# Optimization experiments

Hardware: AMD Instinct MI355X
Metric: run time of the kernel (lower is better)

## Reference

```python
import jax, jax.numpy as jnp
from jax import lax
import numpy as np

HF, WF, CIN, CONV_C, A, STRIDE = 100, 160, 512, 512, 9, 16
NEG = -1e9
IOU_THR = 0.7


def _make_anchor_map(hf, wf, stride):
    # (cy, cx, h, w) per anchor, 9 anchors: scales {64,128,256} x ratios {0.5,1,2}
    cy = (np.arange(hf, dtype=np.float32) + 0.5) * stride
    cx = (np.arange(wf, dtype=np.float32) + 0.5) * stride
    sizes = np.array([[s * np.sqrt(r), s / np.sqrt(r)]
                      for s in (64.0, 128.0, 256.0) for r in (0.5, 1.0, 2.0)],
                     dtype=np.float32)  # [9,2] = (h,w)
    cyg, cxg = np.meshgrid(cy, cx, indexing='ij')  # [hf,wf]
    am = np.zeros((hf, wf, A, 4), np.float32)
    am[..., 0] = cyg[..., None]
    am[..., 1] = cxg[..., None]
    am[..., 2] = sizes[:, 0]
    am[..., 3] = sizes[:, 1]
    return jnp.asarray(am.reshape(1, hf, wf, 4 * A))


def _conv(x, w, b, pad):
    y = lax.conv_general_dilated(x, w, (1, 1), pad,
                                 dimension_numbers=('NHWC', 'HWIO', 'NHWC'))
    return y + b


def _nms(boxes, scores, max_out, iou_thr):
    # jit-friendly fixed-size NMS; index computation is non-differentiable.
    bx = lax.stop_gradient(boxes)
    y1, x1, y2, x2 = bx[:, 0], bx[:, 1], bx[:, 2], bx[:, 3]
    areas = (y2 - y1) * (x2 - x1)

    def step(sc, _):
        best = jnp.argmax(sc)
        ok = sc[best] > NEG * 0.5
        b = bx[best]
        iy1 = jnp.maximum(y1, b[0]); ix1 = jnp.maximum(x1, b[1])
        iy2 = jnp.minimum(y2, b[2]); ix2 = jnp.minimum(x2, b[3])
        inter = jnp.maximum(iy2 - iy1, 0.0) * jnp.maximum(ix2 - ix1, 0.0)
        iou = inter / (areas + areas[best] - inter + 1e-8)
        sc = jnp.where((iou > iou_thr) & ok, NEG, sc)
        sc = sc.at[best].set(NEG)
        return sc, (best, ok)

    _, (keep, valid) = lax.scan(step, lax.stop_gradient(scores), None, length=max_out)
    return jnp.where(valid[:, None], boxes[keep], 0.0)  # [max_out,4], zero-padded


def setup_inputs() -> dict:
    key = jax.random.key(0)
    ks = jax.random.split(key, 6)
    image = jax.random.normal(ks[0], (1, HF * STRIDE, WF * STRIDE, 3), jnp.float32)
    feature_map = jax.random.normal(ks[1], (1, HF, WF, CIN), jnp.float32)
    anchor_map = _make_anchor_map(HF, WF, STRIDE)
    W1 = jax.random.normal(ks[2], (3, 3, CIN, CONV_C), jnp.float32) * 0.01
    b1 = jnp.zeros((CONV_C,), jnp.float32)
    Wc = jax.random.normal(ks[3], (1, 1, CONV_C, A), jnp.float32) * 0.01
    bc = jnp.zeros((A,), jnp.float32)
    Wr = jax.random.normal(ks[4], (1, 1, CONV_C, 4 * A), jnp.float32) * 0.01
    br = jnp.zeros((4 * A,), jnp.float32)
    return {'image': image, 'feature_map': feature_map, 'anchor_map': anchor_map,
            'W1': W1, 'b1': b1, 'Wc': Wc, 'bc': bc, 'Wr': Wr, 'br': br, 'training': 0}


def reference(image, feature_map, anchor_map, W1, b1, Wc, bc, Wr, br, training):
    pre_nms, post_nms = ((12000, 2000) if training else (6000, 300))
    # conv heads
    y = jax.nn.relu(_conv(feature_map, W1, b1, 'SAME'))
    scores_map = jax.nn.softmax(_conv(y, Wc, bc, 'SAME'), axis=-1)   # [1,HF,WF,9]
    delta_map = _conv(y, Wr, br, 'SAME')                              # [1,HF,WF,36]
    # flatten (_extract)
    anchors = anchor_map.reshape(-1, 4)        # (cy,cx,h,w)
    scores = scores_map.reshape(-1)            # [N]
    box_deltas = delta_map.reshape(-1, 4)      # (ty,tx,th,tw)
    # deltas_to_bboxes (means=0, stds=1)
    ctr = anchors[:, :2] + box_deltas[:, :2] * anchors[:, 2:]
    sz = anchors[:, 2:] * jnp.exp(box_deltas[:, 2:])
    proposals = jnp.concatenate([ctr - 0.5 * sz, ctr + 0.5 * sz], axis=1)  # (y1,x1,y2,x2)
    # sort desc + pre-NMS top-k
    top_scores, top_idx = lax.top_k(scores, pre_nms)
    proposals = proposals[top_idx]
    # clip to image
    h = jnp.float32(image.shape[1]); w = jnp.float32(image.shape[2])
    tl = jnp.maximum(proposals[:, 0:2], 0.0)
    y2 = jnp.minimum(proposals[:, 2], h)[:, None]
    x2 = jnp.minimum(proposals[:, 3], w)[:, None]
    proposals = jnp.concatenate([tl, y2, x2], axis=1)
    # size filter (mask instead of gather; NMS skips masked boxes)
    height = proposals[:, 2] - proposals[:, 0]
    width = proposals[:, 3] - proposals[:, 1]
    valid = (height >= 16.0) & (width >= 16.0)
    nms_scores = jnp.where(valid, top_scores, NEG)
    out_props = _nms(proposals, nms_scores, post_nms, IOU_THR)
    return (scores_map, box_deltas, out_props)
```

## Files before the change

kernel.cpp:

```cpp
#include <hip/hip_runtime.h>
#include <math.h>

#define HF 100
#define WFD 160
#define CIN 512
#define CONV_C 512
#define NPIX (HF*WFD)
#define NBOX (NPIX*9)
#define PRE_NMS 6000
#define POST_NMS 300
#define NEGV (-1.0e9f)
#define IMG_H 1600.0f
#define IMG_W 2560.0f
#define NHBINS 32768
#define NWORDS 94
#define NSORT 6016

#define PR 102
#define PC 162
#define NPAD ((size_t)PR*PC*512)

typedef __attribute__((ext_vector_type(8))) _Float16 half8;
typedef __attribute__((ext_vector_type(4))) float floatx4;

__device__ __forceinline__ unsigned short f2h_hi(float x) {
    _Float16 h = (_Float16)x;
    return __builtin_bit_cast(unsigned short, h);
}
__device__ __forceinline__ unsigned short f2h_lo(float x, unsigned short hbits) {
    _Float16 h = __builtin_bit_cast(_Float16, hbits);
    _Float16 l = (_Float16)((x - (float)h) * 2048.0f);
    return __builtin_bit_cast(unsigned short, l);
}

#define GLL16(g, l) __builtin_amdgcn_global_load_lds( \
    (const __attribute__((address_space(1))) void*)(g), \
    (__attribute__((address_space(3))) void*)(l), 16, 0, 0)

static const size_t OYREG = 0;
static const size_t OXH   = OYREG + (size_t)NPIX * CONV_C;
static const size_t OXL   = OXH + NPAD / 2;
static const size_t OWH   = OXL + NPAD / 2;
static const size_t OWL   = OWH + (size_t)9*512*512/2;
static const size_t ORAW  = OWL + (size_t)9*512*512/2;
static const size_t ONMS  = ORAW + NBOX;
static const size_t OPY1  = ONMS + NBOX;
static const size_t OPX1  = OPY1 + NBOX;
static const size_t OPY2  = OPX1 + NBOX;
static const size_t OPX2  = OPY2 + NBOX;
static const size_t OHIST = OPX2 + NBOX;
static const size_t OCNT  = OHIST + NHBINS;
static const size_t OPAR  = OCNT + 4;
static const size_t OCS   = OPAR + 2;
static const size_t OCY1  = OCS + PRE_NMS;
static const size_t OCX1  = OCY1 + PRE_NMS;
static const size_t OCY2  = OCX1 + PRE_NMS;
static const size_t OCX2  = OCY2 + PRE_NMS;
static const size_t OW2H  = OCX2 + PRE_NMS;
static const size_t OW2L  = OW2H + 12288;
static const size_t OMASK = OXH;
static const size_t OSY1  = OXL;
static const size_t OSX1  = OSY1 + NSORT;
static const size_t OSY2  = OSX1 + NSORT;
static const size_t OSX2  = OSY2 + NSORT;
static const size_t OSAR  = OSX2 + NSORT;

__global__ __launch_bounds__(256) void split_x(
    const float* __restrict__ X,
    unsigned short* __restrict__ Xh, unsigned short* __restrict__ Xl)
{
    const int idx = blockIdx.x * 256 + threadIdx.x;
    const int p = idx >> 7;
    const int kq = (idx & 127) * 4;
    const float4 v = *(const float4*)(X + (size_t)p * 512 + kq);
    const int r = p / WFD, c = p % WFD;
    const size_t dst = ((size_t)(r + 1) * PC + (c + 1)) * 512 + kq;
    float vv[4] = { v.x, v.y, v.z, v.w };
    unsigned short h[4], lo[4];
    #pragma unroll
    for (int u = 0; u < 4; ++u) {
        h[u]  = f2h_hi(vv[u]);
        lo[u] = f2h_lo(vv[u], h[u]);
    }
    uint2 ph, pl;
    ph.x = (unsigned)h[0]  | ((unsigned)h[1]  << 16);
    ph.y = (unsigned)h[2]  | ((unsigned)h[3]  << 16);
    pl.x = (unsigned)lo[0] | ((unsigned)lo[1] << 16);
    pl.y = (unsigned)lo[2] | ((unsigned)lo[3] << 16);
    *(uint2*)(Xh + dst) = ph;
    *(uint2*)(Xl + dst) = pl;
}

__global__ __launch_bounds__(256) void split_w(
    const float* __restrict__ W1,
    unsigned short* __restrict__ Wh, unsigned short* __restrict__ Wl)
{
    __shared__ unsigned short Lh[64 * 64];
    __shared__ unsigned short Ll[64 * 64];
    const int t = threadIdx.x;
    const int dydx = blockIdx.x >> 6;
    const int rem  = blockIdx.x & 63;
    const int k0 = (rem >> 3) * 64, n0 = (rem & 7) * 64;

    #pragma unroll
    for (int i = 0; i < 4; ++i) {
        const int f = t + 256 * i;
        const int row = f >> 4;
        const int cp  = (f & 15) * 4;
        const float4 v = *(const float4*)(W1 + ((size_t)(dydx * 512 + k0 + row)) * 512 + n0 + cp);
        float vv[4] = { v.x, v.y, v.z, v.w };
        #pragma unroll
        for (int u = 0; u < 4; ++u) {
            const unsigned short h = f2h_hi(vv[u]);
            Lh[(cp + u) * 64 + row] = h;
            Ll[(cp + u) * 64 + row] = f2h_lo(vv[u], h);
        }
    }
    __syncthreads();
    const int n  = t >> 2;
    const int kp = (t & 3) * 16;
    const size_t gbase = ((size_t)(dydx * 512 + n0 + n)) * 512 + k0 + kp;
    *(uint4*)(Wh + gbase)     = *(const uint4*)(Lh + n * 64 + kp);
    *(uint4*)(Wh + gbase + 8) = *(const uint4*)(Lh + n * 64 + kp + 8);
    *(uint4*)(Wl + gbase)     = *(const uint4*)(Ll + n * 64 + kp);
    *(uint4*)(Wl + gbase + 8) = *(const uint4*)(Ll + n * 64 + kp + 8);
}

__global__ __launch_bounds__(256) void split_w2(
    const float* __restrict__ Wc, const float* __restrict__ Wr,
    unsigned short* __restrict__ W2h, unsigned short* __restrict__ W2l)
{
    const int i = blockIdx.x * 256 + threadIdx.x;
    if (i >= 48 * 512) return;
    const int n = i >> 9, k = i & 511;
    float v = 0.f;
    if (n < 9) v = Wc[k * 9 + n];
    else if (n < 45) v = Wr[k * 36 + (n - 9)];
    const unsigned short h = f2h_hi(v);
    W2h[i] = h;
    W2l[i] = f2h_lo(v, h);
}

__global__ __launch_bounds__(256, 2) void conv_mfma(
    const unsigned short* __restrict__ Xh, const unsigned short* __restrict__ Xl,
    const unsigned short* __restrict__ Wh, const unsigned short* __restrict__ Wl,
    const float* __restrict__ b1,
    unsigned short* __restrict__ Yh, unsigned short* __restrict__ Yl)
{
    __shared__ alignas(16) unsigned short Ah[2][128 * 32];
    __shared__ alignas(16) unsigned short Al[2][128 * 32];
    __shared__ alignas(16) unsigned short Bh[2][128 * 32];
    __shared__ alignas(16) unsigned short Bl[2][128 * 32];

    const int tid = threadIdx.x;
    const int w = tid >> 6, l = tid & 63;
    const int wy = w >> 1, wx = w & 1;

    const int bx = blockIdx.x;
    const int q = bx & 7, s5 = bx >> 3;
    const int tile = (q < 5) ? (q * 16 + s5) : (80 + (q - 5) * 15 + s5);
    const int pm0 = tile * 128, oc0 = blockIdx.y * 128;

    const int swW = ((l & 3) ^ ((l >> 3) & 3)) * 8;
    int aoff[2], boff[2], ldsOff[2];
    #pragma unroll
    for (int i = 0; i < 2; ++i) {
        const int m = w * 32 + i * 16 + (l >> 2);
        const int p = pm0 + m;
        const int r = p / WFD, c = p % WFD;
        aoff[i] = ((r + 1) * PC + (c + 1)) * 512 + swW;
        boff[i] = (oc0 + m) * 512 + swW;
        ldsOff[i] = (w * 32 + i * 16) * 32;
    }

    const int swR = (((l >> 4) ^ ((l >> 1) & 3))) * 8;
    int afrag[4], bfrag[4];
    #pragma unroll
    for (int i = 0; i < 4; ++i) {
        afrag[i] = (wy * 64 + i * 16 + (l & 15)) * 32 + swR;
        bfrag[i] = (wx * 64 + i * 16 + (l & 15)) * 32 + swR;
    }

    floatx4 acc[4][4], accL[4][4];
    #pragma unroll
    for (int j = 0; j < 4; ++j) {
        const float bv = b1[oc0 + wx * 64 + j * 16 + (l & 15)];
        #pragma unroll
        for (int i = 0; i < 4; ++i) {
            acc[i][j][0] = bv; acc[i][j][1] = bv; acc[i][j][2] = bv; acc[i][j][3] = bv;
            accL[i][j][0] = 0.f; accL[i][j][1] = 0.f; accL[i][j][2] = 0.f; accL[i][j][3] = 0.f;
        }
    }

    #define CSTAGE(bf, dAx, dBx)                                    \
        _Pragma("unroll")                                           \
        for (int i = 0; i < 2; ++i) {                               \
            GLL16(Xh + aoff[i] + (dAx), Ah[bf] + ldsOff[i]);        \
            GLL16(Xl + aoff[i] + (dAx), Al[bf] + ldsOff[i]);        \
            GLL16(Wh + boff[i] + (dBx), Bh[bf] + ldsOff[i]);        \
            GLL16(Wl + boff[i] + (dBx), Bl[bf] + ldsOff[i]);        \
        }

    CSTAGE(0, (-PC - 1) * 512, 0);

    for (int step = 0; step < 144; ++step) {
        const int cur = step & 1;
        if (step < 143) {
            const int s1 = step + 1;
            const int d1 = s1 >> 4;
            const int k1 = (s1 & 15) << 5;
            const int dy = d1 / 3 - 1, dx = d1 % 3 - 1;
            CSTAGE(cur ^ 1, (dy * PC + dx) * 512 + k1, d1 * (512 * 512) + k1);
            asm volatile("s_waitcnt vmcnt(8)" ::: "memory");
        } else {
            asm volatile("s_waitcnt vmcnt(0)" ::: "memory");
        }
        __builtin_amdgcn_s_barrier();
        asm volatile("" ::: "memory");

        const unsigned short* Ac = Ah[cur];
        const unsigned short* Lc = Al[cur];
        const unsigned short* Bc = Bh[cur];
        const unsigned short* Mc = Bl[cur];
        half8 fah[4], fal[4], fbh[4], fbl[4];
        #pragma unroll
        for (int i = 0; i < 4; ++i) {
            fah[i] = *(const half8*)(Ac + afrag[i]);
            fal[i] = *(const half8*)(Lc + afrag[i]);
            fbh[i] = *(const half8*)(Bc + bfrag[i]);
            fbl[i] = *(const half8*)(Mc + bfrag[i]);
        }
        #pragma unroll
        for (int i = 0; i < 4; ++i)
            #pragma unroll
            for (int j = 0; j < 4; ++j) {
                acc[i][j]  = __builtin_amdgcn_mfma_f32_16x16x32_f16(fah[i], fbh[j], acc[i][j], 0, 0, 0);
                accL[i][j] = __builtin_amdgcn_mfma_f32_16x16x32_f16(fal[i], fbh[j], accL[i][j], 0, 0, 0);
                accL[i][j] = __builtin_amdgcn_mfma_f32_16x16x32_f16(fah[i], fbl[j], accL[i][j], 0, 0, 0);
            }
        asm volatile("" ::: "memory");
        __builtin_amdgcn_s_barrier();
    }
    #undef CSTAGE

    #pragma unroll
    for (int i = 0; i < 4; ++i) {
        const int row0 = pm0 + wy * 64 + i * 16 + (l >> 4) * 4;
        #pragma unroll
        for (int j = 0; j < 4; ++j) {
            const int col = oc0 + wx * 64 + j * 16 + (l & 15);
            #pragma unroll
            for (int r = 0; r < 4; ++r) {
                const float yv = fmaxf(acc[i][j][r] + accL[i][j][r] * 4.8828125e-4f, 0.f);
                const unsigned short h = f2h_hi(yv);
                const size_t o = (size_t)(row0 + r) * 512 + col;
                Yh[o] = h;
                Yl[o] = f2h_lo(yv, h);
            }
        }
    }
}

__global__ __launch_bounds__(256) void heads_mfma(
    const unsigned short* __restrict__ Yh, const unsigned short* __restrict__ Yl,
    const unsigned short* __restrict__ W2h, const unsigned short* __restrict__ W2l,
    const float* __restrict__ bc, const float* __restrict__ br,
    const float* __restrict__ anch,
    float* __restrict__ out_scores, float* __restrict__ out_deltas,
    float* __restrict__ rawS, float* __restrict__ nmsS,
    float* __restrict__ pY1, float* __restrict__ pX1,
    float* __restrict__ pY2, float* __restrict__ pX2,
    unsigned int* __restrict__ hist)
{
    __shared__ alignas(16) unsigned short Ah[128 * 32];
    __shared__ alignas(16) unsigned short Al[128 * 32];
    __shared__ alignas(16) unsigned short Bh[48 * 32];
    __shared__ alignas(16) unsigned short Bl[48 * 32];
    __shared__ float Lg[128 * 49];
    __shared__ unsigned int Hh[NHBINS / 2];

    const int tid = threadIdx.x;
    const int w = tid >> 6, l = tid & 63;
    const int pm0 = blockIdx.x * 128;

    #pragma unroll 4
    for (int i = tid; i < NHBINS / 2; i += 256) Hh[i] = 0u;

    const int swW = ((l & 3) ^ ((l >> 3) & 3)) * 8;
    int aoff[2], ldsOff[2];
    #pragma unroll
    for (int i = 0; i < 2; ++i) {
        const int m = w * 32 + i * 16 + (l >> 2);
        aoff[i] = (pm0 + m) * 512 + swW;
        ldsOff[i] = (w * 32 + i * 16) * 32;
    }
    const int bglb = (w * 16 + (l >> 2)) * 512 + swW;
    const int blds = w * 16 * 32;

    const int swR = (((l >> 4) ^ ((l >> 1) & 3))) * 8;
    int afrag[2], bfrag[3];
    #pragma unroll
    for (int i = 0; i < 2; ++i)
        afrag[i] = (w * 32 + i * 16 + (l & 15)) * 32 + swR;
    #pragma unroll
    for (int j = 0; j < 3; ++j)
        bfrag[j] = (j * 16 + (l & 15)) * 32 + swR;

    floatx4 acc[2][3], accL[2][3];
    #pragma unroll
    for (int i = 0; i < 2; ++i)
        #pragma unroll
        for (int j = 0; j < 3; ++j) {
            acc[i][j][0] = 0.f; acc[i][j][1] = 0.f; acc[i][j][2] = 0.f; acc[i][j][3] = 0.f;
            accL[i][j] = acc[i][j];
        }

    for (int k0 = 0; k0 < 512; k0 += 32) {
        __syncthreads();
        #pragma unroll
        for (int i = 0; i < 2; ++i) {
            GLL16(Yh + aoff[i] + k0, Ah + ldsOff[i]);
            GLL16(Yl + aoff[i] + k0, Al + ldsOff[i]);
        }
        if (w < 3) {
            GLL16(W2h + bglb + k0, Bh + blds);
            GLL16(W2l + bglb + k0, Bl + blds);
        }
        __syncthreads();
        half8 fah[2], fal[2], fbh[3], fbl[3];
        #pragma unroll
        for (int i = 0; i < 2; ++i) {
            fah[i] = *(const half8*)(Ah + afrag[i]);
            fal[i] = *(const half8*)(Al + afrag[i]);
        }
        #pragma unroll
        for (int j = 0; j < 3; ++j) {
            fbh[j] = *(const half8*)(Bh + bfrag[j]);
            fbl[j] = *(const half8*)(Bl + bfrag[j]);
        }
        #pragma unroll
        for (int i = 0; i < 2; ++i)
            #pragma unroll
            for (int j = 0; j < 3; ++j) {
                acc[i][j]  = __builtin_amdgcn_mfma_f32_16x16x32_f16(fah[i], fbh[j], acc[i][j], 0, 0, 0);
                accL[i][j] = __builtin_amdgcn_mfma_f32_16x16x32_f16(fal[i], fbh[j], accL[i][j], 0, 0, 0);
                accL[i][j] = __builtin_amdgcn_mfma_f32_16x16x32_f16(fah[i], fbl[j], accL[i][j], 0, 0, 0);
            }
    }

    __syncthreads();
    #pragma unroll
    for (int i = 0; i < 2; ++i) {
        const int prow0 = w * 32 + i * 16 + (l >> 4) * 4;
        #pragma unroll
        for (int j = 0; j < 3; ++j) {
            const int col = j * 16 + (l & 15);
            #pragma unroll
            for (int r = 0; r < 4; ++r)
                Lg[(prow0 + r) * 49 + col] = acc[i][j][r] + accL[i][j][r] * 4.8828125e-4f;
        }
    }
    __syncthreads();

    if (tid < 128) {
        const int p = pm0 + tid;
        float ac[9], arr[36];
        #pragma unroll
        for (int a = 0; a < 9; ++a) ac[a] = Lg[tid * 49 + a] + bc[a];
        #pragma unroll
        for (int j = 0; j < 36; ++j) arr[j] = Lg[tid * 49 + 9 + j] + br[j];

        float m = ac[0];
        #pragma unroll
        for (int a = 1; a < 9; ++a) m = fmaxf(m, ac[a]);
        float s = 0.f, e[9];
        #pragma unroll
        for (int a = 0; a < 9; ++a) { e[a] = expf(ac[a] - m); s += e[a]; }
        #pragma unroll
        for (int a = 0; a < 9; ++a) e[a] = e[a] / s;

        #pragma unroll
        for (int a = 0; a < 9; ++a) out_scores[p * 9 + a] = e[a];
        #pragma unroll
        for (int a = 0; a < 9; ++a)
            *(float4*)(out_deltas + (size_t)p * 36 + 4 * a) =
                make_float4(arr[4*a], arr[4*a+1], arr[4*a+2], arr[4*a+3]);

        #pragma unroll
        for (int a = 0; a < 9; ++a) {
            const float4 an = *(const float4*)(anch + (size_t)p * 36 + 4 * a);
            const float cty = an.x + arr[4*a]   * an.z;
            const float ctx = an.y + arr[4*a+1] * an.w;
            const float szy = an.z * expf(arr[4*a+2]);
            const float szx = an.w * expf(arr[4*a+3]);
            float y1 = fmaxf(cty - 0.5f * szy, 0.f);
            float x1 = fmaxf(ctx - 0.5f * szx, 0.f);
            float y2 = fminf(cty + 0.5f * szy, IMG_H);
            float x2 = fminf(ctx + 0.5f * szx, IMG_W);
            const bool valid = ((y2 - y1) >= 16.f) && ((x2 - x1) >= 16.f);
            const int idx = p * 9 + a;
            rawS[idx] = e[a];
            nmsS[idx] = valid ? e[a] : NEGV;
            pY1[idx] = y1; pX1[idx] = x1; pY2[idx] = y2; pX2[idx] = x2;
            const unsigned b = __float_as_uint(e[a]) >> 15;
            atomicAdd(&Hh[b >> 1], (b & 1) ? 65536u : 1u);
        }
    }

    __syncthreads();
    for (int i = tid; i < NHBINS / 2; i += 256) {
        const unsigned v = Hh[i];
        if (v) {
            const unsigned lo = v & 0xFFFFu;
            const unsigned hi = v >> 16;
            if (lo) atomicAdd(&hist[2 * i],     lo);
            if (hi) atomicAdd(&hist[2 * i + 1], hi);
        }
    }
}

__global__ __launch_bounds__(1024) void select_k(const unsigned int* __restrict__ hist,
                                                 int* __restrict__ params)
{
    __shared__ unsigned int ps[1024];
    const int t = threadIdx.x;
    unsigned int loc[32];
    unsigned int sum = 0;
    #pragma unroll 4
    for (int i = 0; i < 32; ++i) { loc[i] = hist[t * 32 + i]; sum += loc[i]; }
    ps[t] = sum;
    for (int off = 1; off < 1024; off <<= 1) {
        __syncthreads();
        const unsigned int add = (t + off < 1024) ? ps[t + off] : 0u;
        __syncthreads();
        ps[t] += add;
    }
    __syncthreads();
    const unsigned int above = (t < 1023) ? ps[t + 1] : 0u;
    if (above < (unsigned)PRE_NMS && ps[t] >= (unsigned)PRE_NMS) {
        unsigned int cum = above;
        for (int j = 31; j >= 0; --j) {
            const unsigned int h = loc[j];
            if (cum + h >= (unsigned)PRE_NMS) {
                params[0] = t * 32 + j;
                params[1] = PRE_NMS - (int)cum;
                break;
            }
            cum += h;
        }
    }
}

__global__ void compact_k(const float* __restrict__ rawS, const float* __restrict__ nmsS,
                          const float* __restrict__ pY1, const float* __restrict__ pX1,
                          const float* __restrict__ pY2, const float* __restrict__ pX2,
                          const int* __restrict__ params, int* __restrict__ cnts,
                          float* __restrict__ cS,
                          float* __restrict__ cY1, float* __restrict__ cX1,
                          float* __restrict__ cY2, float* __restrict__ cX2)
{
    const int i = blockIdx.x * 256 + threadIdx.x;
    const int lane = threadIdx.x & 63;
    const bool act = i < NBOX;
    int b = -1;
    if (act) b = (int)(__float_as_uint(rawS[i]) >> 15);
    const int bin = params[0];
    const int need = params[1];
    int pos = -1;

    {
        const bool p = act && (b > bin);
        const unsigned long long m = __ballot(p);
        if (p) {
            const int leader = __ffsll(m) - 1;
            int base = 0;
            if (lane == leader) base = atomicAdd(&cnts[0], __popcll(m));
            base = __shfl(base, leader, 64);
            pos = base + __popcll(m & ((1ULL << lane) - 1));
        }
    }
    {
        const bool p = act && (b == bin);
        const unsigned long long m = __ballot(p);
        if (p) {
            const int leader = __ffsll(m) - 1;
            int base2 = 0;
            if (lane == leader) base2 = atomicAdd(&cnts[1], __popcll(m));
            base2 = __shfl(base2, leader, 64);
            const int t2 = base2 + __popcll(m & ((1ULL << lane) - 1));
            const bool take = t2 < need;
            const unsigned long long m3 = __ballot(take);
            if (take) {
                const int leader3 = __ffsll(m3) - 1;
                int base3 = 0;
                if (lane == leader3) base3 = atomicAdd(&cnts[0], __popcll(m3));
                base3 = __shfl(base3, leader3, 64);
                pos = base3 + __popcll(m3 & ((1ULL << lane) - 1));
            }
        }
    }

    if (pos >= 0) {
        const float sv = nmsS[i];
        cS[pos]  = sv;
        cY1[pos] = pY1[i]; cX1[pos] = pX1[i];
        cY2[pos] = pY2[i]; cX2[pos] = pX2[i];
        if (sv > NEGV * 0.5f) atomicAdd(&cnts[2], 1);
    }
}

__global__ __launch_bounds__(1024) void sort_k(
    const float* __restrict__ cS,
    const float* __restrict__ cY1, const float* __restrict__ cX1,
    const float* __restrict__ cY2, const float* __restrict__ cX2,
    float* __restrict__ sY1, float* __restrict__ sX1,
    float* __restrict__ sY2, float* __restrict__ sX2,
    float* __restrict__ sAr)
{
    __shared__ unsigned long long keys[8192];
    const int t = threadIdx.x;
    for (int i = t; i < 8192; i += 1024) {
        unsigned long long k;
        if (i < PRE_NMS) {
            const unsigned b = __float_as_uint(cS[i]);
            const unsigned m = (b & 0x80000000u) ? ~b : (b | 0x80000000u);
            k = ((unsigned long long)(~m) << 32) | (unsigned)i;
        } else {
            k = ~0ULL;
        }
        keys[i] = k;
    }
    for (int kk = 2; kk <= 8192; kk <<= 1) {
        for (int j = kk >> 1; j > 0; j >>= 1) {
            __syncthreads();
            for (int t4 = t; t4 < 4096; t4 += 1024) {
                const int i  = ((t4 & ~(j - 1)) << 1) | (t4 & (j - 1));
                const int p2 = i | j;
                const bool up = ((i & kk) == 0);
                const unsigned long long a = keys[i], b = keys[p2];
                const bool sw = up ? (a > b) : (a < b);
                if (sw) { keys[i] = b; keys[p2] = a; }
            }
        }
    }
    __syncthreads();
    for (int i = t; i < NSORT; i += 1024) {
        if (i < PRE_NMS) {
            const int j = (int)(keys[i] & 0xFFFFFFFFu);
            const float y1 = cY1[j], x1 = cX1[j], y2 = cY2[j], x2 = cX2[j];
            sY1[i] = y1; sX1[i] = x1; sY2[i] = y2; sX2[i] = x2;
            sAr[i] = (y2 - y1) * (x2 - x1);
        } else {
            sY1[i] = 0.f; sX1[i] = 0.f; sY2[i] = 0.f; sX2[i] = 0.f; sAr[i] = 0.f;
        }
    }
}

__global__ __launch_bounds__(64) void mask_k(
    const float* __restrict__ sY1, const float* __restrict__ sX1,
    const float* __restrict__ sY2, const float* __restrict__ sX2,
    const float* __restrict__ sAr, unsigned long long* __restrict__ mask)
{
    __shared__ float ly1[64], lx1[64], ly2[64], lx2[64], lar[64];
    const int t = threadIdx.x;
    const int c = blockIdx.y * 64 + t;
    ly1[t] = sY1[c]; lx1[t] = sX1[c]; ly2[t] = sY2[c]; lx2[t] = sX2[c]; lar[t] = sAr[c];
    __syncthreads();
    const int r = blockIdx.x * 64 + t;
    const float ry1 = sY1[r], rx1 = sX1[r], ry2 = sY2[r], rx2 = sX2[r], rar = sAr[r];
    unsigned long long bits = 0ULL;
    #pragma unroll 8
    for (int u = 0; u < 64; ++u) {
        const float iy1 = fmaxf(ry1, ly1[u]);
        const float ix1 = fmaxf(rx1, lx1[u]);
        const float iy2 = fminf(ry2, ly2[u]);
        const float ix2 = fminf(rx2, lx2[u]);
        const float inter = fmaxf(iy2 - iy1, 0.f) * fmaxf(ix2 - ix1, 0.f);
        const float iou = inter / (lar[u] + rar - inter + 1e-8f);
        bits |= (iou > 0.7f) ? (1ULL << u) : 0ULL;
    }
    mask[(size_t)r * NWORDS + blockIdx.y] = bits;
}

__global__ __launch_bounds__(256) void scan2_k(
    const float* __restrict__ sY1, const float* __restrict__ sX1,
    const float* __restrict__ sY2, const float* __restrict__ sX2,
    const unsigned long long* __restrict__ mask, const int* __restrict__ cnts,
    float* __restrict__ outP)
{
    __shared__ alignas(16) unsigned long long rows[2][64][96];
    __shared__ int sn;
    const int tid = threadIdx.x;
    const int wv = tid >> 6, l = tid & 63;
    const int nvRaw = cnts[2];
    const int nv = nvRaw < PRE_NMS ? nvRaw : PRE_NMS;
    const int nw = (nv + 63) >> 6;
    unsigned long long r0 = 0ULL, r1 = 0ULL;
    int n = 0;
    if (tid == 0) sn = 0;

    #define SSTAGE(w_, buf_)                                                     \
        for (int r = 0; r < 16; ++r) {                                           \
            if (l < 47)                                                          \
                GLL16(mask + (size_t)(((w_) << 6) + wv * 16 + r) * NWORDS + 2*l, \
                      &rows[buf_][wv * 16 + r][0]);                              \
        }

    if (nw > 0) { SSTAGE(0, 0); }

    for (int w = 0; w < nw; ++w) {
        const int buf = w & 1;
        const bool pf = (w + 1 < nw);
        if (pf) {
            SSTAGE(w + 1, buf ^ 1);
            asm volatile("s_waitcnt vmcnt(16)" ::: "memory");
        } else {
            asm volatile("s_waitcnt vmcnt(0)" ::: "memory");
        }
        __syncthreads();

        if (wv == 0) {
            const int base = w << 6;
            const int ci = base + l;
            const float v1 = sY1[ci], v2 = sX1[ci], v3 = sY2[ci], v4 = sX2[ci];
            unsigned long long cw = (w < 64) ? __shfl(r0, w, 64) : __shfl(r1, w - 64, 64);
            const int lim = nv - base;
            if (lim < 64) cw |= (~0ULL << lim);
            while (cw != ~0ULL && n < POST_NMS) {
                const int b = (int)__builtin_ctzll(~cw);
                const float by1 = __shfl(v1, b, 64);
                const float bx1 = __shfl(v2, b, 64);
                const float by2 = __shfl(v3, b, 64);
                const float bx2 = __shfl(v4, b, 64);
                if (l == 0) {
                    outP[4 * n + 0] = by1; outP[4 * n + 1] = bx1;
                    outP[4 * n + 2] = by2; outP[4 * n + 3] = bx2;
                }
                ++n;
                cw |= (1ULL << b);
                if (n >= POST_NMS) break;
                r0 |= rows[buf][b][l];
                if (l < NWORDS - 64) r1 |= rows[buf][b][64 + l];
                cw |= rows[buf][b][w];
            }
            if (l == 0) sn = n;
        }
        __syncthreads();
        n = sn;
        if (n >= POST_NMS) break;
    }
    #undef SSTAGE
    asm volatile("s_waitcnt vmcnt(0)" ::: "memory");

    for (int idx = 4 * n + tid; idx < 4 * POST_NMS; idx += 256) outP[idx] = 0.f;
}

extern "C" void kernel_launch(void* const* d_in, const int* in_sizes, int n_in,
                              void* d_out, int out_size, void* d_ws, size_t ws_size,
                              hipStream_t stream)
{
    const float* X    = (const float*)d_in[1];
    const float* anch = (const float*)d_in[2];
    const float* W1   = (const float*)d_in[3];
    const float* b1   = (const float*)d_in[4];
    const float* Wc   = (const float*)d_in[5];
    const float* bc   = (const float*)d_in[6];
    const float* Wr   = (const float*)d_in[7];
    const float* br   = (const float*)d_in[8];

    float* out = (float*)d_out;
    float* ws  = (float*)d_ws;

    unsigned short* Yh = (unsigned short*)(ws + OYREG);
    unsigned short* Yl = Yh + (size_t)NPIX * CONV_C;
    unsigned short* Xh = (unsigned short*)(ws + OXH);
    unsigned short* Xl = (unsigned short*)(ws + OXL);
    unsigned short* Wh = (unsigned short*)(ws + OWH);
    unsigned short* Wl = (unsigned short*)(ws + OWL);
    float* rawS = ws + ORAW;
    float* nmsS = ws + ONMS;
    float* pY1  = ws + OPY1;
    float* pX1  = ws + OPX1;
    float* pY2  = ws + OPY2;
    float* pX2  = ws + OPX2;
    unsigned int* hist = (unsigned int*)(ws + OHIST);
    int* cnts   = (int*)(ws + OCNT);
    int* params = (int*)(ws + OPAR);
    float* cS   = ws + OCS;
    float* cY1  = ws + OCY1;
    float* cX1  = ws + OCX1;
    float* cY2  = ws + OCY2;
    float* cX2  = ws + OCX2;
    unsigned short* W2h = (unsigned short*)(ws + OW2H);
    unsigned short* W2l = (unsigned short*)(ws + OW2L);
    float* sY1  = ws + OSY1;
    float* sX1  = ws + OSX1;
    float* sY2  = ws + OSY2;
    float* sX2  = ws + OSX2;
    float* sAr  = ws + OSAR;
    unsigned long long* mask = (unsigned long long*)(ws + OMASK);

    float* out_scores = out;
    float* out_deltas = out + NBOX;
    float* out_props  = out + (size_t)NBOX * 5;

    hipMemsetAsync(hist, 0, (NHBINS + 8) * sizeof(unsigned int), stream);
    hipMemsetAsync(Xh, 0, 2 * NPAD * sizeof(unsigned short), stream);

    split_x<<<8000, 256, 0, stream>>>(X, Xh, Xl);
    split_w<<<576, 256, 0, stream>>>(W1, Wh, Wl);
    split_w2<<<96, 256, 0, stream>>>(Wc, Wr, W2h, W2l);

    conv_mfma<<<dim3(125, 4), 256, 0, stream>>>(Xh, Xl, Wh, Wl, b1, Yh, Yl);

    heads_mfma<<<125, 256, 0, stream>>>(Yh, Yl, W2h, W2l, bc, br, anch,
        out_scores, out_deltas, rawS, nmsS, pY1, pX1, pY2, pX2, hist);

    select_k<<<1, 1024, 0, stream>>>(hist, params);
    compact_k<<<(NBOX + 255) / 256, 256, 0, stream>>>(
        rawS, nmsS, pY1, pX1, pY2, pX2, params, cnts, cS, cY1, cX1, cY2, cX2);

    sort_k<<<1, 1024, 0, stream>>>(cS, cY1, cX1, cY2, cX2,
                                   sY1, sX1, sY2, sX2, sAr);
    mask_k<<<dim3(NWORDS, NWORDS), 64, 0, stream>>>(sY1, sX1, sY2, sX2, sAr, mask);
    scan2_k<<<1, 256, 0, stream>>>(sY1, sX1, sY2, sX2, mask, cnts, out_props);
}
```

Before: 641.5 us.

## Enlarge conv tile to 256x128 with 512-thread blocks and XCD-aware mapping

```diff
diff --git a/kernel.cpp b/kernel.cpp
--- a/kernel.cpp
+++ b/kernel.cpp
@@ -141,14 +141,14 @@
     W2l[i] = f2h_lo(v, h);
 }
 
-__global__ __launch_bounds__(256, 2) void conv_mfma(
+__global__ __launch_bounds__(512, 1) void conv_mfma(
     const unsigned short* __restrict__ Xh, const unsigned short* __restrict__ Xl,
     const unsigned short* __restrict__ Wh, const unsigned short* __restrict__ Wl,
     const float* __restrict__ b1,
     unsigned short* __restrict__ Yh, unsigned short* __restrict__ Yl)
 {
-    __shared__ alignas(16) unsigned short Ah[2][128 * 32];
-    __shared__ alignas(16) unsigned short Al[2][128 * 32];
+    __shared__ alignas(16) unsigned short Ah[2][256 * 32];
+    __shared__ alignas(16) unsigned short Al[2][256 * 32];
     __shared__ alignas(16) unsigned short Bh[2][128 * 32];
     __shared__ alignas(16) unsigned short Bl[2][128 * 32];
 
@@ -156,22 +156,25 @@
     const int w = tid >> 6, l = tid & 63;
     const int wy = w >> 1, wx = w & 1;
 
-    const int bx = blockIdx.x;
-    const int q = bx & 7, s5 = bx >> 3;
-    const int tile = (q < 5) ? (q * 16 + s5) : (80 + (q - 5) * 15 + s5);
-    const int pm0 = tile * 128, oc0 = blockIdx.y * 128;
+    const int L = blockIdx.x;
+    const int xcd = L & 7;
+    const int oc0 = (xcd >> 1) * 128;
+    const int tile = ((L >> 3) << 1) | (xcd & 1);
+    const int pm0 = tile * 256;
 
     const int swW = ((l & 3) ^ ((l >> 3) & 3)) * 8;
-    int aoff[2], boff[2], ldsOff[2];
+    int aoff[2], ldsOffA[2];
     #pragma unroll
     for (int i = 0; i < 2; ++i) {
         const int m = w * 32 + i * 16 + (l >> 2);
         const int p = pm0 + m;
         const int r = p / WFD, c = p % WFD;
         aoff[i] = ((r + 1) * PC + (c + 1)) * 512 + swW;
-        boff[i] = (oc0 + m) * 512 + swW;
-        ldsOff[i] = (w * 32 + i * 16) * 32;
-    }
+        ldsOffA[i] = (w * 32 + i * 16) * 32;
+    }
+    const int mB = w * 16 + (l >> 2);
+    const int boff = (oc0 + mB) * 512 + swW;
+    const int ldsOffB = (w * 16) * 32;
 
     const int swR = (((l >> 4) ^ ((l >> 1) & 3))) * 8;
     int afrag[4], bfrag[4];
@@ -195,11 +198,11 @@
     #define CSTAGE(bf, dAx, dBx)                                    \
         _Pragma("unroll")                                           \
         for (int i = 0; i < 2; ++i) {                               \
-            GLL16(Xh + aoff[i] + (dAx), Ah[bf] + ldsOff[i]);        \
-            GLL16(Xl + aoff[i] + (dAx), Al[bf] + ldsOff[i]);        \
-            GLL16(Wh + boff[i] + (dBx), Bh[bf] + ldsOff[i]);        \
-            GLL16(Wl + boff[i] + (dBx), Bl[bf] + ldsOff[i]);        \
-        }
+            GLL16(Xh + aoff[i] + (dAx), Ah[bf] + ldsOffA[i]);       \
+            GLL16(Xl + aoff[i] + (dAx), Al[bf] + ldsOffA[i]);       \
+        }                                                           \
+        GLL16(Wh + boff + (dBx), Bh[bf] + ldsOffB);                 \
+        GLL16(Wl + boff + (dBx), Bl[bf] + ldsOffB);
 
     CSTAGE(0, (-PC - 1) * 512, 0);
 
@@ -211,7 +214,7 @@
             const int k1 = (s1 & 15) << 5;
             const int dy = d1 / 3 - 1, dx = d1 % 3 - 1;
             CSTAGE(cur ^ 1, (dy * PC + dx) * 512 + k1, d1 * (512 * 512) + k1);
-            asm volatile("s_waitcnt vmcnt(8)" ::: "memory");
+            asm volatile("s_waitcnt vmcnt(6)" ::: "memory");
         } else {
             asm volatile("s_waitcnt vmcnt(0)" ::: "memory");
         }
@@ -251,11 +254,14 @@
             const int col = oc0 + wx * 64 + j * 16 + (l & 15);
             #pragma unroll
             for (int r = 0; r < 4; ++r) {
-                const float yv = fmaxf(acc[i][j][r] + accL[i][j][r] * 4.8828125e-4f, 0.f);
-                const unsigned short h = f2h_hi(yv);
-                const size_t o = (size_t)(row0 + r) * 512 + col;
-                Yh[o] = h;
-                Yl[o] = f2h_lo(yv, h);
+                const int row = row0 + r;
+                if (row < NPIX) {
+                    const float yv = fmaxf(acc[i][j][r] + accL[i][j][r] * 4.8828125e-4f, 0.f);
+                    const unsigned short h = f2h_hi(yv);
+                    const size_t o = (size_t)row * 512 + col;
+                    Yh[o] = h;
+                    Yl[o] = f2h_lo(yv, h);
+                }
             }
         }
     }
@@ -711,7 +717,7 @@
     split_w<<<576, 256, 0, stream>>>(W1, Wh, Wl);
     split_w2<<<96, 256, 0, stream>>>(Wc, Wr, W2h, W2l);
 
-    conv_mfma<<<dim3(125, 4), 256, 0, stream>>>(Xh, Xl, Wh, Wl, b1, Yh, Yl);
+    conv_mfma<<<256, 512, 0, stream>>>(Xh, Xl, Wh, Wl, b1, Yh, Yl);
 
     heads_mfma<<<125, 256, 0, stream>>>(Yh, Yl, W2h, W2l, bc, br, anch,
         out_scores, out_deltas, rawS, nmsS, pY1, pX1, pY2, pX2, hist);
```

Result: no change. 653.9 us (+1.9%).

## Replace bitonic sort of pre-NMS candidates with LDS radix sort

Applied to the files above, without the earlier changes.

```diff
diff --git a/kernel.cpp b/kernel.cpp
--- a/kernel.cpp
+++ b/kernel.cpp
@@ -517,36 +517,92 @@
     float* __restrict__ sY2, float* __restrict__ sX2,
     float* __restrict__ sAr)
 {
-    __shared__ unsigned long long keys[8192];
+    __shared__ unsigned long long A[6144];
+    __shared__ unsigned long long B[6144];
+    __shared__ unsigned int wsum[16 * 16];
+    __shared__ unsigned int dtot[16];
+    __shared__ unsigned int gb[16 * 16];
     const int t = threadIdx.x;
-    for (int i = t; i < 8192; i += 1024) {
+    const int w = t >> 6, lane = t & 63;
+
+    for (int i = t; i < 6144; i += 1024) {
         unsigned long long k;
         if (i < PRE_NMS) {
-            const unsigned b = __float_as_uint(cS[i]);
-            const unsigned m = (b & 0x80000000u) ? ~b : (b | 0x80000000u);
+            const unsigned bb = __float_as_uint(cS[i]);
+            const unsigned m = (bb & 0x80000000u) ? ~bb : (bb | 0x80000000u);
             k = ((unsigned long long)(~m) << 32) | (unsigned)i;
         } else {
-            k = ~0ULL;
-        }
-        keys[i] = k;
-    }
-    for (int kk = 2; kk <= 8192; kk <<= 1) {
-        for (int j = kk >> 1; j > 0; j >>= 1) {
-            __syncthreads();
-            for (int t4 = t; t4 < 4096; t4 += 1024) {
-                const int i  = ((t4 & ~(j - 1)) << 1) | (t4 & (j - 1));
-                const int p2 = i | j;
-                const bool up = ((i & kk) == 0);
-                const unsigned long long a = keys[i], b = keys[p2];
-                const bool sw = up ? (a > b) : (a < b);
-                if (sw) { keys[i] = b; keys[p2] = a; }
+            k = 0xFFFFFFFF00000000ULL | (unsigned)i;
+        }
+        A[i] = k;
+    }
+    __syncthreads();
+
+    unsigned long long* src = A;
+    unsigned long long* dst = B;
+    #pragma unroll 1
+    for (int p = 0; p < 8; ++p) {
+        const int sh = 32 + p * 4;
+        const int b6 = t * 6;
+        const unsigned long long e0 = src[b6+0], e1 = src[b6+1], e2 = src[b6+2],
+                                 e3 = src[b6+3], e4 = src[b6+4], e5 = src[b6+5];
+        const int d0 = (int)((e0 >> sh) & 15);
+        const int d1 = (int)((e1 >> sh) & 15);
+        const int d2 = (int)((e2 >> sh) & 15);
+        const int d3 = (int)((e3 >> sh) & 15);
+        const int d4 = (int)((e4 >> sh) & 15);
+        const int d5 = (int)((e5 >> sh) & 15);
+        const int r1 = (d1==d0);
+        const int r2 = (d2==d0)+(d2==d1);
+        const int r3 = (d3==d0)+(d3==d1)+(d3==d2);
+        const int r4 = (d4==d0)+(d4==d1)+(d4==d2)+(d4==d3);
+        const int r5 = (d5==d0)+(d5==d1)+(d5==d2)+(d5==d3)+(d5==d4);
+
+        int exclv[16];
+        #pragma unroll
+        for (int v = 0; v < 16; ++v) {
+            const int c = (d0==v)+(d1==v)+(d2==v)+(d3==v)+(d4==v)+(d5==v);
+            int s = c;
+            #pragma unroll
+            for (int o = 1; o < 64; o <<= 1) {
+                const int u = __shfl_up(s, (unsigned)o, 64);
+                if (lane >= o) s += u;
             }
-        }
-    }
-    __syncthreads();
+            exclv[v] = s - c;
+            if (lane == 63) wsum[v * 16 + w] = (unsigned)s;
+        }
+        __syncthreads();
+        if (t < 16) {
+            unsigned s2 = 0;
+            for (int w2 = 0; w2 < 16; ++w2) s2 += wsum[t * 16 + w2];
+            dtot[t] = s2;
+        }
+        __syncthreads();
+        if (t < 256) {
+            const int v = t >> 4, ww = t & 15;
+            unsigned bs = 0;
+            for (int v2 = 0; v2 < v; ++v2) bs += dtot[v2];
+            for (int w2 = 0; w2 < ww; ++w2) bs += wsum[v * 16 + w2];
+            gb[t] = bs;
+        }
+        __syncthreads();
+        #pragma unroll
+        for (int v = 0; v < 16; ++v) {
+            const int myb = (int)gb[v * 16 + w] + exclv[v];
+            if (d0 == v) dst[myb]      = e0;
+            if (d1 == v) dst[myb + r1] = e1;
+            if (d2 == v) dst[myb + r2] = e2;
+            if (d3 == v) dst[myb + r3] = e3;
+            if (d4 == v) dst[myb + r4] = e4;
+            if (d5 == v) dst[myb + r5] = e5;
+        }
+        __syncthreads();
+        unsigned long long* tmp = src; src = dst; dst = tmp;
+    }
+
     for (int i = t; i < NSORT; i += 1024) {
         if (i < PRE_NMS) {
-            const int j = (int)(keys[i] & 0xFFFFFFFFu);
+            const int j = (int)(src[i] & 0xFFFFFFFFu);
             const float y1 = cY1[j], x1 = cX1[j], y2 = cY2[j], x2 = cX2[j];
             sY1[i] = y1; sX1[i] = x1; sY2[i] = y2; sX2[i] = x2;
             sAr[i] = (y2 - y1) * (x2 - x1);
```

Result: slower. 659.7 us (+2.8%).
